# Performance work log

Hardware: AMD Instinct MI355X
Metric: run time of the kernel (lower is better)

Reference implementation:

```python
import jax, jax.numpy as jnp
import numpy as np

THRESHOLD = 0.5


def setup_inputs() -> dict:
    key = jax.random.key(0)
    k1, k2 = jax.random.split(key)
    N, D = 8192, 4096
    x = jax.random.normal(k1, (N, D), dtype=jnp.float32)
    gate_w = jax.random.normal(k2, (D, 2), dtype=jnp.float32) * (1.0 / np.sqrt(D))
    gate_b = jnp.zeros((2,), dtype=jnp.float32)
    return {"x": x, "gate_w": gate_w, "gate_b": gate_b}


def reference(x, gate_w, gate_b):
    # gate: [N, D] @ [D, 2] -> [N, 2] scores in [0, 1]
    score = jax.nn.sigmoid(x @ gate_w + gate_b)
    # threshold protocol: token routed to branch i iff score[:, i] > 0.5
    # (dispatch_score=False -> routed payload is x itself)
    m0 = score[:, 0:1] > THRESHOLD  # [N, 1]
    m1 = score[:, 1:2] > THRESHOLD  # [N, 1]
    zero = jnp.zeros((), dtype=x.dtype)
    x0 = jnp.where(m0, x, zero)  # expert1 = Identity on routed rows
    x1 = jnp.where(m1, x, zero)  # expert2 = Identity on routed rows
    # combine fabric: sum branch outputs back at original token positions
    combined = x0 + x1
    return (x0, x1, combined)
```

## Files before the change

### kernel.cpp

```cpp
#include <hip/hip_runtime.h>


typedef float f32x4 __attribute__((ext_vector_type(4)));

template <int K>
__global__ __launch_bounds__(256) void branch_route_kernel(
    const float* __restrict__ x,
    const float* __restrict__ gw,
    const float* __restrict__ gb,
    float* __restrict__ out,
    int N, int D)
{
    const int row = blockIdx.x;
    const int t = threadIdx.x;
    const long long rowbase = (long long)row * D;

    f32x4 xs[K];
    float d0 = 0.f, d1 = 0.f;

#pragma unroll
    for (int k = 0; k < K; ++k) {
        const int idx = (t + k * 256) * 4;
        const f32x4 xv = *reinterpret_cast<const f32x4*>(x + rowbase + idx);
        const f32x4 wa = *reinterpret_cast<const f32x4*>(gw + 2 * idx);
        const f32x4 wb = *reinterpret_cast<const f32x4*>(gw + 2 * idx + 4);
        xs[k] = xv;
        d0 += xv.x * wa.x + xv.y * wa.z + xv.z * wb.x + xv.w * wb.z;
        d1 += xv.x * wa.y + xv.y * wa.w + xv.z * wb.y + xv.w * wb.w;
    }

#pragma unroll
    for (int off = 32; off > 0; off >>= 1) {
        d0 += __shfl_down(d0, off, 64);
        d1 += __shfl_down(d1, off, 64);
    }
    __shared__ float s0[4], s1[4];
    const int wave = t >> 6;
    if ((t & 63) == 0) { s0[wave] = d0; s1[wave] = d1; }
    __syncthreads();
    const float tot0 = s0[0] + s0[1] + s0[2] + s0[3] + gb[0];
    const float tot1 = s1[0] + s1[1] + s1[2] + s1[3] + gb[1];

    const float m0 = (tot0 > 0.f) ? 1.f : 0.f;
    const float m1 = (tot1 > 0.f) ? 1.f : 0.f;
    const float mc = m0 + m1;

    float* __restrict__ out0 = out;
    float* __restrict__ out1 = out + (long long)N * D;
    float* __restrict__ out2 = out + 2LL * (long long)N * D;

#pragma unroll
    for (int k = 0; k < K; ++k) {
        const int idx = (t + k * 256) * 4;
        const f32x4 xv = xs[k];
        const f32x4 a = xv * m0;
        const f32x4 b = xv * m1;
        const f32x4 c = xv * mc;
        *reinterpret_cast<f32x4*>(out0 + rowbase + idx) = a;
        *reinterpret_cast<f32x4*>(out1 + rowbase + idx) = b;
        *reinterpret_cast<f32x4*>(out2 + rowbase + idx) = c;
    }
}

extern "C" void kernel_launch(void* const* d_in, const int* in_sizes, int n_in,
                              void* d_out, int out_size, void* d_ws, size_t ws_size,
                              hipStream_t stream) {
    const float* x  = (const float*)d_in[0];
    const float* gw = (const float*)d_in[1];
    const float* gb = (const float*)d_in[2];
    float* out = (float*)d_out;

    const int D = in_sizes[1] / 2;
    const int N = in_sizes[0] / D;

    dim3 grid(N), block(256);
    const int K = D / (256 * 4);
    switch (K) {
        case 1: branch_route_kernel<1><<<grid, block, 0, stream>>>(x, gw, gb, out, N, D); break;
        case 2: branch_route_kernel<2><<<grid, block, 0, stream>>>(x, gw, gb, out, N, D); break;
        case 4: branch_route_kernel<4><<<grid, block, 0, stream>>>(x, gw, gb, out, N, D); break;
        case 8: branch_route_kernel<8><<<grid, block, 0, stream>>>(x, gw, gb, out, N, D); break;
        default: break;
    }
}
```

Baseline: 484.5 us.

## Split fused gate-and-route kernel into separate gate and apply kernels

Splits the single kernel into a gate kernel that computes per-row masks into workspace and an apply kernel that rereads x and writes the three outputs. The aim is to drop the K-vector register cache of x and the dependency between the reduction and the stores, so the store-heavy pass can run at higher occupancy. In exchange, x (128 MB) is read twice from global memory, plus there is an extra launch and a small mask round-trip.

```diff
diff --git a/kernel.cpp b/kernel.cpp
--- a/kernel.cpp
+++ b/kernel.cpp
@@ -2,29 +2,27 @@
 
 
 typedef float f32x4 __attribute__((ext_vector_type(4)));
+typedef float f32x2 __attribute__((ext_vector_type(2)));
 
 template <int K>
-__global__ __launch_bounds__(256) void branch_route_kernel(
+__global__ __launch_bounds__(256) void gate_kernel(
     const float* __restrict__ x,
     const float* __restrict__ gw,
     const float* __restrict__ gb,
-    float* __restrict__ out,
-    int N, int D)
+    float* __restrict__ masks,
+    int D)
 {
     const int row = blockIdx.x;
     const int t = threadIdx.x;
     const long long rowbase = (long long)row * D;
 
-    f32x4 xs[K];
     float d0 = 0.f, d1 = 0.f;
-
 #pragma unroll
     for (int k = 0; k < K; ++k) {
         const int idx = (t + k * 256) * 4;
         const f32x4 xv = *reinterpret_cast<const f32x4*>(x + rowbase + idx);
         const f32x4 wa = *reinterpret_cast<const f32x4*>(gw + 2 * idx);
         const f32x4 wb = *reinterpret_cast<const f32x4*>(gw + 2 * idx + 4);
-        xs[k] = xv;
         d0 += xv.x * wa.x + xv.y * wa.z + xv.z * wb.x + xv.w * wb.z;
         d1 += xv.x * wa.y + xv.y * wa.w + xv.z * wb.y + xv.w * wb.w;
     }
@@ -38,27 +36,41 @@
     const int wave = t >> 6;
     if ((t & 63) == 0) { s0[wave] = d0; s1[wave] = d1; }
     __syncthreads();
-    const float tot0 = s0[0] + s0[1] + s0[2] + s0[3] + gb[0];
-    const float tot1 = s1[0] + s1[1] + s1[2] + s1[3] + gb[1];
+    if (t == 0) {
+        const float tot0 = s0[0] + s0[1] + s0[2] + s0[3] + gb[0];
+        const float tot1 = s1[0] + s1[1] + s1[2] + s1[3] + gb[1];
+        f32x2 mm;
+        mm.x = (tot0 > 0.f) ? 1.f : 0.f;
+        mm.y = (tot1 > 0.f) ? 1.f : 0.f;
+        *reinterpret_cast<f32x2*>(masks + 2 * row) = mm;
+    }
+}
 
-    const float m0 = (tot0 > 0.f) ? 1.f : 0.f;
-    const float m1 = (tot1 > 0.f) ? 1.f : 0.f;
-    const float mc = m0 + m1;
+template <int K>
+__global__ __launch_bounds__(256) void apply_kernel(
+    const float* __restrict__ x,
+    const float* __restrict__ masks,
+    float* __restrict__ out,
+    long long ND, int D)
+{
+    const int row = blockIdx.x;
+    const int t = threadIdx.x;
+    const long long rowbase = (long long)row * D;
+
+    const f32x2 mm = *reinterpret_cast<const f32x2*>(masks + 2 * row);
+    const float m0 = mm.x, m1 = mm.y, mc = mm.x + mm.y;
 
     float* __restrict__ out0 = out;
-    float* __restrict__ out1 = out + (long long)N * D;
-    float* __restrict__ out2 = out + 2LL * (long long)N * D;
+    float* __restrict__ out1 = out + ND;
+    float* __restrict__ out2 = out + 2 * ND;
 
 #pragma unroll
     for (int k = 0; k < K; ++k) {
         const int idx = (t + k * 256) * 4;
-        const f32x4 xv = xs[k];
-        const f32x4 a = xv * m0;
-        const f32x4 b = xv * m1;
-        const f32x4 c = xv * mc;
-        *reinterpret_cast<f32x4*>(out0 + rowbase + idx) = a;
-        *reinterpret_cast<f32x4*>(out1 + rowbase + idx) = b;
-        *reinterpret_cast<f32x4*>(out2 + rowbase + idx) = c;
+        const f32x4 xv = *reinterpret_cast<const f32x4*>(x + rowbase + idx);
+        *reinterpret_cast<f32x4*>(out0 + rowbase + idx) = xv * m0;
+        *reinterpret_cast<f32x4*>(out1 + rowbase + idx) = xv * m1;
+        *reinterpret_cast<f32x4*>(out2 + rowbase + idx) = xv * mc;
     }
 }
 
@@ -69,17 +81,31 @@
     const float* gw = (const float*)d_in[1];
     const float* gb = (const float*)d_in[2];
     float* out = (float*)d_out;
+    float* masks = (float*)d_ws;
 
     const int D = in_sizes[1] / 2;
     const int N = in_sizes[0] / D;
+    const long long ND = (long long)N * D;
 
     dim3 grid(N), block(256);
     const int K = D / (256 * 4);
     switch (K) {
-        case 1: branch_route_kernel<1><<<grid, block, 0, stream>>>(x, gw, gb, out, N, D); break;
-        case 2: branch_route_kernel<2><<<grid, block, 0, stream>>>(x, gw, gb, out, N, D); break;
-        case 4: branch_route_kernel<4><<<grid, block, 0, stream>>>(x, gw, gb, out, N, D); break;
-        case 8: branch_route_kernel<8><<<grid, block, 0, stream>>>(x, gw, gb, out, N, D); break;
+        case 1:
+            gate_kernel<1><<<grid, block, 0, stream>>>(x, gw, gb, masks, D);
+            apply_kernel<1><<<grid, block, 0, stream>>>(x, masks, out, ND, D);
+            break;
+        case 2:
+            gate_kernel<2><<<grid, block, 0, stream>>>(x, gw, gb, masks, D);
+            apply_kernel<2><<<grid, block, 0, stream>>>(x, masks, out, ND, D);
+            break;
+        case 4:
+            gate_kernel<4><<<grid, block, 0, stream>>>(x, gw, gb, masks, D);
+            apply_kernel<4><<<grid, block, 0, stream>>>(x, masks, out, ND, D);
+            break;
+        case 8:
+            gate_kernel<8><<<grid, block, 0, stream>>>(x, gw, gb, masks, D);
+            apply_kernel<8><<<grid, block, 0, stream>>>(x, masks, out, ND, D);
+            break;
         default: break;
     }
 }
```

Result: slower. 509.1 us (+5.1%).
